# Performance work log

Measured on AMD Instinct MI355X. Metric: run time of the kernel, lower is better.

The kernel has to match this reference:

```python
import jax, jax.numpy as jnp
import numpy as np

EPS = 1e-5


def conv1x1(x, w, b):
    # x: [b,c,h,w], w: [o,c], b: [o] -> [b,o,h,w]  (1x1 conv == channel matmul)
    return jnp.einsum('bchw,oc->bohw', x, w) + b[None, :, None, None]


def nor_mean_std(x):
    # instance norm over spatial dims (torch calc_mean_std uses unbiased var)
    mean = jnp.mean(x, axis=(2, 3), keepdims=True)
    var = jnp.var(x, axis=(2, 3), keepdims=True, ddof=1)
    return (x - mean) / jnp.sqrt(var + EPS)


def nor_mean(x):
    mean = jnp.mean(x, axis=(2, 3), keepdims=True)
    return x - mean, mean


def net(x, w1, b1, w2, b2):
    return conv1x1(jax.nn.relu(conv1x1(x, w1, b1)), w2, b2)


def setup_inputs() -> dict:
    key = jax.random.key(0)
    ks = jax.random.split(key, 8)
    B, C, H, W = 8, 256, 128, 128
    return {
        'content': jax.random.normal(ks[0], (B, C, H, W), jnp.float32),
        'style': jax.random.normal(ks[1], (B, C, H, W), jnp.float32),
        'w1': jax.random.normal(ks[2], (128, 256), jnp.float32) * 0.05,
        'b1': jax.random.normal(ks[3], (128,), jnp.float32) * 0.05,
        'w2': jax.random.normal(ks[4], (32, 128), jnp.float32) * 0.05,
        'b2': jax.random.normal(ks[5], (32,), jnp.float32) * 0.05,
        'wu': jax.random.normal(ks[6], (256, 32), jnp.float32) * 0.05,
        'bu': jax.random.normal(ks[7], (256,), jnp.float32) * 0.05,
    }


def reference(content, style, w1, b1, w2, b2, wu, bu):
    cF_nor = nor_mean_std(content)
    sF_nor, smean = nor_mean(style)
    cF = net(cF_nor, w1, b1, w2, b2)          # [b,32,h,w]
    sF = net(sF_nor, w1, b1, w2, b2)          # [b,32,h,w]
    b, c, h, w = cF.shape
    hw = h * w
    sf = sF.reshape(b, c, hw)
    # channel covariance: [b,32,32]
    s_cov = jnp.einsum('bcn,bdn->bcd', sf, sf) / hw
    s_cov = jax.nn.softmax(s_cov, axis=-1) * (c ** -0.5)
    gF = jnp.einsum('bcd,bdn->bcn', s_cov, cF.reshape(b, c, hw)).reshape(b, c, h, w)
    gF = conv1x1(gF, wu, bu)                  # [b,256,h,w]
    return gF + smean + content
```

## Files before the change

kernel.cpp:

```cpp
#include <hip/hip_runtime.h>

#define HW 16384
#define C_IN 256
#define C_MID 128
#define C_OUT 32
#define EPSF 1e-5f

typedef __bf16 bf16x8 __attribute__((ext_vector_type(8)));
typedef __bf16 bf16x4 __attribute__((ext_vector_type(4)));
typedef float f32x4 __attribute__((ext_vector_type(4)));

__device__ __forceinline__ bf16x4 cvt4(f32x4 v) {
    bf16x4 r;
    r[0] = (__bf16)v[0]; r[1] = (__bf16)v[1];
    r[2] = (__bf16)v[2]; r[3] = (__bf16)v[3];
    return r;
}

__global__ __launch_bounds__(512) void k_stats_s(const float* __restrict__ style,
                                                 float* __restrict__ smean,
                                                 __bf16* __restrict__ sbf) {
    const int bc = blockIdx.x;
    const int t = threadIdx.x;
    const f32x4* sp = (const f32x4*)(style + (size_t)bc * HW);
    const int phase = (bc * 257) & 4095;

    int idx[8];
    #pragma unroll
    for (int i = 0; i < 8; ++i) idx[i] = (phase + t + i * 512) & 4095;

    f32x4 s[8];
    #pragma unroll
    for (int i = 0; i < 8; ++i) s[i] = __builtin_nontemporal_load(sp + idx[i]);
    asm volatile("" ::
        "v"(s[0]), "v"(s[1]), "v"(s[2]), "v"(s[3]),
        "v"(s[4]), "v"(s[5]), "v"(s[6]), "v"(s[7]));

    {
        bf16x4* sb = (bf16x4*)(sbf + (size_t)bc * HW);
        #pragma unroll
        for (int i = 0; i < 8; ++i) sb[idx[i]] = cvt4(s[i]);
    }

    f32x4 a01 = s[0] + s[1], a23 = s[2] + s[3], a45 = s[4] + s[5], a67 = s[6] + s[7];
    f32x4 a = (a01 + a23) + (a45 + a67);
    float ss = (a[0] + a[1]) + (a[2] + a[3]);

    #pragma unroll
    for (int d = 32; d > 0; d >>= 1) ss += __shfl_xor(ss, d, 64);
    __shared__ float rss[8];
    const int wv = t >> 6;
    if ((t & 63) == 0) rss[wv] = ss;
    __syncthreads();
    if (t == 0) {
        float S = 0.f;
        #pragma unroll
        for (int i = 0; i < 8; ++i) S += rss[i];
        smean[bc] = S / (float)HW;
    }
}

__global__ __launch_bounds__(512) void k_stats_c(const float* __restrict__ content,
                                                 float* __restrict__ cmean,
                                                 float* __restrict__ crstd,
                                                 __bf16* __restrict__ cbf) {
    const int bc = blockIdx.x;
    const int t = threadIdx.x;
    const f32x4* cp = (const f32x4*)(content + (size_t)bc * HW);
    const int phase = (bc * 257) & 4095;

    int idx[8];
    #pragma unroll
    for (int i = 0; i < 8; ++i) idx[i] = (phase + t + i * 512) & 4095;

    f32x4 c[8];
    #pragma unroll
    for (int i = 0; i < 8; ++i) c[i] = __builtin_nontemporal_load(cp + idx[i]);
    asm volatile("" ::
        "v"(c[0]), "v"(c[1]), "v"(c[2]), "v"(c[3]),
        "v"(c[4]), "v"(c[5]), "v"(c[6]), "v"(c[7]));

    {
        bf16x4* cb = (bf16x4*)(cbf + (size_t)bc * HW);
        #pragma unroll
        for (int i = 0; i < 8; ++i) cb[idx[i]] = cvt4(c[i]);
    }

    f32x4 a01 = c[0] + c[1], a23 = c[2] + c[3], a45 = c[4] + c[5], a67 = c[6] + c[7];
    f32x4 a = (a01 + a23) + (a45 + a67);
    float cs = (a[0] + a[1]) + (a[2] + a[3]);
    f32x4 q01 = c[0]*c[0] + c[1]*c[1], q23 = c[2]*c[2] + c[3]*c[3];
    f32x4 q45 = c[4]*c[4] + c[5]*c[5], q67 = c[6]*c[6] + c[7]*c[7];
    f32x4 q = (q01 + q23) + (q45 + q67);
    float cq = (q[0] + q[1]) + (q[2] + q[3]);

    #pragma unroll
    for (int d = 32; d > 0; d >>= 1) {
        cs += __shfl_xor(cs, d, 64);
        cq += __shfl_xor(cq, d, 64);
    }
    __shared__ float rs[8], rq[8];
    const int wv = t >> 6;
    if ((t & 63) == 0) { rs[wv] = cs; rq[wv] = cq; }
    __syncthreads();
    if (t == 0) {
        float S = 0.f, Q = 0.f;
        #pragma unroll
        for (int i = 0; i < 8; ++i) { S += rs[i]; Q += rq[i]; }
        float n = (float)HW;
        float var = (Q - S * S / n) / (n - 1.f);
        cmean[bc] = S / n;
        crstd[bc] = 1.f / sqrtf(var + EPSF);
    }
}

__global__ __launch_bounds__(256) void k_wprep_s(const float* __restrict__ w1,
                                                 const float* __restrict__ b1,
                                                 const float* __restrict__ w2,
                                                 const float* __restrict__ smean,
                                                 __bf16* __restrict__ W1s,
                                                 float* __restrict__ bias1s,
                                                 __bf16* __restrict__ W2b) {
    int o = blockIdx.x, b = blockIdx.y, t = threadIdx.x;
    float w = w1[o * 256 + t];
    if (b == 0) {
        W1s[o * 256 + t] = (__bf16)w;
        if (t < 32) W2b[o * 32 + t] = (__bf16)w2[o * 32 + t];
    }
    float ps = w * smean[b * 256 + t];
    __shared__ float rB[256];
    rB[t] = ps;
    __syncthreads();
    for (int off = 128; off > 0; off >>= 1) {
        if (t < off) rB[t] += rB[t + off];
        __syncthreads();
    }
    if (t == 0) bias1s[b * 128 + o] = b1[o] - rB[0];
}

__global__ __launch_bounds__(256) void k_wprep_c(const float* __restrict__ w1,
                                                 const float* __restrict__ b1,
                                                 const float* __restrict__ cmean,
                                                 const float* __restrict__ crstd,
                                                 __bf16* __restrict__ W1c,
                                                 float* __restrict__ bias1c) {
    int o = blockIdx.x, b = blockIdx.y, t = threadIdx.x;
    float w = w1[o * 256 + t];
    float r = crstd[b * 256 + t];
    float wc = w * r;
    W1c[((size_t)(b * 128 + o)) * 256 + t] = (__bf16)wc;
    float pc = wc * cmean[b * 256 + t];
    __shared__ float rA[256];
    rA[t] = pc;
    __syncthreads();
    for (int off = 128; off > 0; off >>= 1) {
        if (t < off) rA[t] += rA[t + off];
        __syncthreads();
    }
    if (t == 0) bias1c[b * 128 + o] = b1[o] - rA[0];
}

__device__ __forceinline__ void stage_tile(const __bf16* __restrict__ xb,
                                           int p0, int tid, __bf16* Xl) {
    const int c = tid;
    const __bf16* src = xb + (size_t)c * HW + p0;
    bf16x8 v[8];
    #pragma unroll
    for (int j = 0; j < 8; ++j) v[j] = *(const bf16x8*)(src + j * 8);
    char* base = (char*)Xl;
    #pragma unroll
    for (int j = 0; j < 8; ++j) {
        #pragma unroll
        for (int e = 0; e < 8; ++e)
            *(__bf16*)(base + (j * 8 + e) * 512 + ((2 * c) ^ (e << 4))) = v[j][e];
    }
}

__global__ __launch_bounds__(256) void k_net_s(const __bf16* __restrict__ x,
                                               const __bf16* __restrict__ W1,
                                               const float* __restrict__ bias1,
                                               const __bf16* __restrict__ W2,
                                               const float* __restrict__ b2,
                                               float* __restrict__ partial) {
    __shared__ __bf16 Xl[64 * 256];
    __shared__ __bf16 Tl[64 * 128];
    const int tid = threadIdx.x;
    const int l = tid & 63, wv = tid >> 6;
    const int lr = l & 15, g = l >> 4;
    const int sw = (lr & 7) << 4;
    const int p0 = blockIdx.x * 64;
    const int b = blockIdx.y;
    const __bf16* xb = x + (size_t)b * C_IN * HW;

    stage_tile(xb, p0, tid, Xl);
    __syncthreads();

    const f32x4 zero4 = {0.f, 0.f, 0.f, 0.f};
    f32x4 acc[2][4];
    #pragma unroll
    for (int mt = 0; mt < 2; ++mt)
        #pragma unroll
        for (int nt = 0; nt < 4; ++nt) acc[mt][nt] = zero4;

    const __bf16* wrow0 = W1 + (size_t)(wv * 32 + lr) * 256 + g * 8;
    const __bf16* wrow1 = wrow0 + 16 * 256;

    #pragma unroll
    for (int kt = 0; kt < 8; ++kt) {
        bf16x8 a0 = *(const bf16x8*)(wrow0 + kt * 32);
        bf16x8 a1 = *(const bf16x8*)(wrow1 + kt * 32);
        #pragma unroll
        for (int nt = 0; nt < 4; ++nt) {
            const char* xrow = (const char*)&Xl[(nt * 16 + lr) * 256];
            bf16x8 bfr = *(const bf16x8*)(xrow + (((kt * 32 + g * 8) * 2) ^ sw));
            acc[0][nt] = __builtin_amdgcn_mfma_f32_16x16x32_bf16(a0, bfr, acc[0][nt], 0, 0, 0);
            acc[1][nt] = __builtin_amdgcn_mfma_f32_16x16x32_bf16(a1, bfr, acc[1][nt], 0, 0, 0);
        }
    }

    float4 bia[2];
    bia[0] = *(const float4*)&bias1[b * 128 + wv * 32 + g * 4];
    bia[1] = *(const float4*)&bias1[b * 128 + wv * 32 + 16 + g * 4];
    __syncthreads();
    #pragma unroll
    for (int mt = 0; mt < 2; ++mt) {
        #pragma unroll
        for (int nt = 0; nt < 4; ++nt) {
            const int p = nt * 16 + lr;
            char* trow = (char*)&Tl[p * 128];
            const int ob = (wv * 32 + mt * 16 + g * 4) * 2;
            bf16x4 tv;
            tv[0] = (__bf16)fmaxf(acc[mt][nt][0] + bia[mt].x, 0.f);
            tv[1] = (__bf16)fmaxf(acc[mt][nt][1] + bia[mt].y, 0.f);
            tv[2] = (__bf16)fmaxf(acc[mt][nt][2] + bia[mt].z, 0.f);
            tv[3] = (__bf16)fmaxf(acc[mt][nt][3] + bia[mt].w, 0.f);
            *(bf16x4*)(trow + (ob ^ sw)) = tv;
        }
    }
    __syncthreads();

    f32x4 acc2[2];
    acc2[0] = zero4; acc2[1] = zero4;
    const int p = wv * 16 + lr;
    const char* trow = (const char*)&Tl[p * 128];
    const __bf16* w2r0 = W2 + (size_t)lr * 128 + g * 8;
    const __bf16* w2r1 = w2r0 + 16 * 128;
    #pragma unroll
    for (int kt = 0; kt < 4; ++kt) {
        bf16x8 bfr = *(const bf16x8*)(trow + (((kt * 32 + g * 8) * 2) ^ sw));
        bf16x8 a0 = *(const bf16x8*)(w2r0 + kt * 32);
        bf16x8 a1 = *(const bf16x8*)(w2r1 + kt * 32);
        acc2[0] = __builtin_amdgcn_mfma_f32_16x16x32_bf16(a0, bfr, acc2[0], 0, 0, 0);
        acc2[1] = __builtin_amdgcn_mfma_f32_16x16x32_bf16(a1, bfr, acc2[1], 0, 0, 0);
    }
    float4 bb0 = *(const float4*)&b2[g * 4];
    float4 bb1 = *(const float4*)&b2[16 + g * 4];
    const int o0 = g * 4;

    float* gt = (float*)Xl;
    gt[(o0 + 0) * 65 + p] = acc2[0][0] + bb0.x;
    gt[(o0 + 1) * 65 + p] = acc2[0][1] + bb0.y;
    gt[(o0 + 2) * 65 + p] = acc2[0][2] + bb0.z;
    gt[(o0 + 3) * 65 + p] = acc2[0][3] + bb0.w;
    gt[(16 + o0 + 0) * 65 + p] = acc2[1][0] + bb1.x;
    gt[(16 + o0 + 1) * 65 + p] = acc2[1][1] + bb1.y;
    gt[(16 + o0 + 2) * 65 + p] = acc2[1][2] + bb1.z;
    gt[(16 + o0 + 3) * 65 + p] = acc2[1][3] + bb1.w;
    __syncthreads();
    const int gi = tid >> 3, jb = (tid & 7) * 4;
    float g4[4] = {0.f, 0.f, 0.f, 0.f};
    #pragma unroll 8
    for (int n = 0; n < 64; ++n) {
        float si = gt[gi * 65 + n];
        #pragma unroll
        for (int q = 0; q < 4; ++q)
            g4[q] = fmaf(si, gt[(jb + q) * 65 + n], g4[q]);
    }
    float* dst = partial + ((size_t)(b * 256 + blockIdx.x)) * 1024 + tid * 4;
    #pragma unroll
    for (int q = 0; q < 4; ++q) dst[q] = g4[q];
}

__global__ __launch_bounds__(1024) void k_softmax2(const float* __restrict__ partial,
                                                   float* __restrict__ scov) {
    int b = blockIdx.x;
    int j = threadIdx.x, i = threadIdx.y;
    const float* base = partial + (size_t)b * 256 * 1024 + i * 32 + j;
    float v0 = 0.f, v1 = 0.f, v2 = 0.f, v3 = 0.f;
    #pragma unroll 4
    for (int s = 0; s < 256; s += 4) {
        v0 += base[(s + 0) * 1024];
        v1 += base[(s + 1) * 1024];
        v2 += base[(s + 2) * 1024];
        v3 += base[(s + 3) * 1024];
    }
    float v = ((v0 + v1) + (v2 + v3)) * (1.f / (float)HW);
    float m = v;
    #pragma unroll
    for (int d = 16; d > 0; d >>= 1) m = fmaxf(m, __shfl_xor(m, d, 32));
    float e = expf(v - m);
    float sum = e;
    #pragma unroll
    for (int d = 16; d > 0; d >>= 1) sum += __shfl_xor(sum, d, 32);
    scov[(size_t)b * 1024 + i * 32 + j] = e / sum * 0.17677669529663687f;
}

__global__ __launch_bounds__(256) void k_netc_final(const __bf16* __restrict__ x,
                                                    const __bf16* __restrict__ W1,
                                                    const float* __restrict__ bias1,
                                                    const __bf16* __restrict__ W2,
                                                    const float* __restrict__ b2,
                                                    const float* __restrict__ scov,
                                                    const float* __restrict__ wu,
                                                    const float* __restrict__ bu,
                                                    const float* __restrict__ smean,
                                                    float* __restrict__ out) {
    __shared__ __bf16 Xl[64 * 256];
    __shared__ __bf16 Tl[64 * 128];
    __shared__ float sCov[1024];
    __shared__ float sG[32 * 64];
    const int tid = threadIdx.x;
    const int l = tid & 63, wv = tid >> 6;
    const int lr = l & 15, g = l >> 4;
    const int sw = (lr & 7) << 4;
    const int p0 = blockIdx.x * 64;
    const int b = blockIdx.y;
    const __bf16* xb = x + (size_t)b * C_IN * HW;

    #pragma unroll
    for (int q = 0; q < 4; ++q)
        sCov[tid + 256 * q] = scov[(size_t)b * 1024 + tid + 256 * q];
    stage_tile(xb, p0, tid, Xl);
    __syncthreads();

    const f32x4 zero4 = {0.f, 0.f, 0.f, 0.f};
    f32x4 acc1[2][4];
    #pragma unroll
    for (int mt = 0; mt < 2; ++mt)
        #pragma unroll
        for (int nt = 0; nt < 4; ++nt) acc1[mt][nt] = zero4;

    const __bf16* W1b = W1 + ((size_t)b << 15);
    const __bf16* wrow0 = W1b + (size_t)(wv * 32 + lr) * 256 + g * 8;
    const __bf16* wrow1 = wrow0 + 16 * 256;

    #pragma unroll
    for (int kt = 0; kt < 8; ++kt) {
        bf16x8 a0 = *(const bf16x8*)(wrow0 + kt * 32);
        bf16x8 a1 = *(const bf16x8*)(wrow1 + kt * 32);
        #pragma unroll
        for (int nt = 0; nt < 4; ++nt) {
            const char* xrow = (const char*)&Xl[(nt * 16 + lr) * 256];
            bf16x8 bfr = *(const bf16x8*)(xrow + (((kt * 32 + g * 8) * 2) ^ sw));
            acc1[0][nt] = __builtin_amdgcn_mfma_f32_16x16x32_bf16(a0, bfr, acc1[0][nt], 0, 0, 0);
            acc1[1][nt] = __builtin_amdgcn_mfma_f32_16x16x32_bf16(a1, bfr, acc1[1][nt], 0, 0, 0);
        }
    }

    float4 bia[2];
    bia[0] = *(const float4*)&bias1[b * 128 + wv * 32 + g * 4];
    bia[1] = *(const float4*)&bias1[b * 128 + wv * 32 + 16 + g * 4];
    #pragma unroll
    for (int mt = 0; mt < 2; ++mt) {
        #pragma unroll
        for (int nt = 0; nt < 4; ++nt) {
            const int p = nt * 16 + lr;
            char* trow = (char*)&Tl[p * 128];
            const int ob = (wv * 32 + mt * 16 + g * 4) * 2;
            bf16x4 tv;
            tv[0] = (__bf16)fmaxf(acc1[mt][nt][0] + bia[mt].x, 0.f);
            tv[1] = (__bf16)fmaxf(acc1[mt][nt][1] + bia[mt].y, 0.f);
            tv[2] = (__bf16)fmaxf(acc1[mt][nt][2] + bia[mt].z, 0.f);
            tv[3] = (__bf16)fmaxf(acc1[mt][nt][3] + bia[mt].w, 0.f);
            *(bf16x4*)(trow + (ob ^ sw)) = tv;
        }
    }
    __syncthreads();

    f32x4 acc2[2];
    acc2[0] = zero4; acc2[1] = zero4;
    const int p = wv * 16 + lr;
    {
        const char* trow = (const char*)&Tl[p * 128];
        const __bf16* w2r0 = W2 + (size_t)lr * 128 + g * 8;
        const __bf16* w2r1 = w2r0 + 16 * 128;
        #pragma unroll
        for (int kt = 0; kt < 4; ++kt) {
            bf16x8 bfr = *(const bf16x8*)(trow + (((kt * 32 + g * 8) * 2) ^ sw));
            bf16x8 a0 = *(const bf16x8*)(w2r0 + kt * 32);
            bf16x8 a1 = *(const bf16x8*)(w2r1 + kt * 32);
            acc2[0] = __builtin_amdgcn_mfma_f32_16x16x32_bf16(a0, bfr, acc2[0], 0, 0, 0);
            acc2[1] = __builtin_amdgcn_mfma_f32_16x16x32_bf16(a1, bfr, acc2[1], 0, 0, 0);
        }
    }
    float4 bb0 = *(const float4*)&b2[g * 4];
    float4 bb1 = *(const float4*)&b2[16 + g * 4];
    const int o0 = g * 4;

    __syncthreads();
    float* sC = (float*)Tl;
    sC[(o0 + 0) * 64 + p] = acc2[0][0] + bb0.x;
    sC[(o0 + 1) * 64 + p] = acc2[0][1] + bb0.y;
    sC[(o0 + 2) * 64 + p] = acc2[0][2] + bb0.z;
    sC[(o0 + 3) * 64 + p] = acc2[0][3] + bb0.w;
    sC[(16 + o0 + 0) * 64 + p] = acc2[1][0] + bb1.x;
    sC[(16 + o0 + 1) * 64 + p] = acc2[1][1] + bb1.y;
    sC[(16 + o0 + 2) * 64 + p] = acc2[1][2] + bb1.z;
    sC[(16 + o0 + 3) * 64 + p] = acc2[1][3] + bb1.w;
    __syncthreads();

    {
        int gp = tid & 63, gib = (tid >> 6) * 8;
        #pragma unroll
        for (int rr = 0; rr < 8; ++rr) {
            int gi = gib + rr;
            float a = 0.f;
            #pragma unroll
            for (int k = 0; k < 32; ++k)
                a = fmaf(sCov[gi * 32 + k], sC[k * 64 + gp], a);
            sG[gi * 64 + gp] = a;
        }
    }
    __syncthreads();

    const int tx = tid & 7, ty = tid >> 3;
    const float* wurow = wu + (size_t)(ty * 8) * 32;
    float acc[8][8];
    #pragma unroll
    for (int i = 0; i < 8; ++i)
        #pragma unroll
        for (int j = 0; j < 8; ++j) acc[i][j] = 0.f;
    #pragma unroll 4
    for (int k = 0; k < 32; ++k) {
        float a[8];
        #pragma unroll
        for (int i = 0; i < 8; ++i) a[i] = wurow[i * 32 + k];
        float4 b4a = *(const float4*)&sG[k * 64 + tx * 8];
        float4 b4b = *(const float4*)&sG[k * 64 + tx * 8 + 4];
        float bb[8] = {b4a.x, b4a.y, b4a.z, b4a.w, b4b.x, b4b.y, b4b.z, b4b.w};
        #pragma unroll
        for (int i = 0; i < 8; ++i)
            #pragma unroll
            for (int j = 0; j < 8; ++j)
                acc[i][j] = fmaf(a[i], bb[j], acc[i][j]);
    }
    float cvv[8][8];
    #pragma unroll
    for (int j = 0; j < 8; ++j) {
        const int pl = tx * 8 + j;
        bf16x8 rv = *(const bf16x8*)((const char*)Xl + pl * 512 + ((ty * 16) ^ (j << 4)));
        #pragma unroll
        for (int i = 0; i < 8; ++i) cvv[i][j] = (float)rv[i];
    }
    #pragma unroll
    for (int i = 0; i < 8; ++i) {
        int o = ty * 8 + i;
        float add = bu[o] + smean[b * 256 + o];
        float* dst = out + (size_t)b * C_IN * HW + (size_t)o * HW + p0 + tx * 8;
        f32x4 r0 = {acc[i][0] + add + cvv[i][0], acc[i][1] + add + cvv[i][1],
                    acc[i][2] + add + cvv[i][2], acc[i][3] + add + cvv[i][3]};
        f32x4 r1 = {acc[i][4] + add + cvv[i][4], acc[i][5] + add + cvv[i][5],
                    acc[i][6] + add + cvv[i][6], acc[i][7] + add + cvv[i][7]};
        __builtin_nontemporal_store(r0, (f32x4*)dst);
        __builtin_nontemporal_store(r1, (f32x4*)(dst + 4));
    }
}

extern "C" void kernel_launch(void* const* d_in, const int* in_sizes, int n_in,
                              void* d_out, int out_size, void* d_ws, size_t ws_size,
                              hipStream_t stream) {
    const float* content = (const float*)d_in[0];
    const float* style   = (const float*)d_in[1];
    const float* w1      = (const float*)d_in[2];
    const float* b1      = (const float*)d_in[3];
    const float* w2      = (const float*)d_in[4];
    const float* b2      = (const float*)d_in[5];
    const float* wu      = (const float*)d_in[6];
    const float* bu      = (const float*)d_in[7];
    float* out = (float*)d_out;
    float* ws  = (float*)d_ws;

    float* cmean   = ws;
    float* crstd   = ws + 2048;
    float* smean   = ws + 4096;
    float* scov    = ws + 6144;
    float* bias1c  = ws + 14336;
    float* bias1s  = ws + 15360;
    __bf16* W2b    = (__bf16*)(ws + 16384);
    __bf16* W1s    = (__bf16*)(ws + 18432);
    __bf16* W1c    = (__bf16*)(ws + 34816);
    float* partial = ws + 165888;
    __bf16* cbf    = (__bf16*)(ws + 2263040);
    __bf16* sbf    = (__bf16*)(ws + 19040256);

    k_stats_s<<<dim3(2048), 512, 0, stream>>>(style, smean, sbf);
    k_wprep_s<<<dim3(128, 8), 256, 0, stream>>>(w1, b1, w2, smean, W1s, bias1s, W2b);
    k_net_s<<<dim3(256, 8), 256, 0, stream>>>(sbf, W1s, bias1s, W2b, b2, partial);
    k_softmax2<<<dim3(8), dim3(32, 32), 0, stream>>>(partial, scov);
    k_stats_c<<<dim3(2048), 512, 0, stream>>>(content, cmean, crstd, cbf);
    k_wprep_c<<<dim3(128, 8), 256, 0, stream>>>(w1, b1, cmean, crstd, W1c, bias1c);
    k_netc_final<<<dim3(256, 8), 256, 0, stream>>>(cbf, W1c, bias1c, W2b, b2,
                                                   scov, wu, bu, smean, out);
}
```

Measured before the change: 225.9 us.

## Double-buffer K-chunked input tiles in final kernel to cut LDS and overlap loads

The fused final kernel no longer stages the whole 64x256 bf16 input tile in shared memory. It streams 64-channel chunks through two 8 KB buffers, prefetching the next chunk into registers while MFMAs run on the current one. That drops shared memory to about 45 KB, and launch bounds now request 3 blocks per CU to raise occupancy. The residual add rereads the bf16 input from global memory instead of shared memory. The costs are extra barriers per chunk, 16 scalar 2-byte transposing shared stores per thread, and a second global read of the tile.

```diff
diff --git a/kernel.cpp b/kernel.cpp
--- a/kernel.cpp
+++ b/kernel.cpp
@@ -305,20 +305,23 @@
     scov[(size_t)b * 1024 + i * 32 + j] = e / sum * 0.17677669529663687f;
 }
 
-__global__ __launch_bounds__(256) void k_netc_final(const __bf16* __restrict__ x,
-                                                    const __bf16* __restrict__ W1,
-                                                    const float* __restrict__ bias1,
-                                                    const __bf16* __restrict__ W2,
-                                                    const float* __restrict__ b2,
-                                                    const float* __restrict__ scov,
-                                                    const float* __restrict__ wu,
-                                                    const float* __restrict__ bu,
-                                                    const float* __restrict__ smean,
-                                                    float* __restrict__ out) {
-    __shared__ __bf16 Xl[64 * 256];
-    __shared__ __bf16 Tl[64 * 128];
-    __shared__ float sCov[1024];
-    __shared__ float sG[32 * 64];
+__global__ __launch_bounds__(256, 3) void k_netc_final(const __bf16* __restrict__ x,
+                                                       const __bf16* __restrict__ W1,
+                                                       const float* __restrict__ bias1,
+                                                       const __bf16* __restrict__ W2,
+                                                       const float* __restrict__ b2,
+                                                       const float* __restrict__ scov,
+                                                       const float* __restrict__ wu,
+                                                       const float* __restrict__ bu,
+                                                       const float* __restrict__ smean,
+                                                       float* __restrict__ out) {
+    __shared__ char smem[45056];
+    __bf16* Xb[2] = {(__bf16*)smem, (__bf16*)(smem + 8192)};
+    __bf16* Tl  = (__bf16*)(smem + 16384);
+    float* sCov = (float*)(smem + 32768);
+    float* sG   = (float*)(smem + 36864);
+    float* sC   = (float*)(smem + 16384);
+
     const int tid = threadIdx.x;
     const int l = tid & 63, wv = tid >> 6;
     const int lr = l & 15, g = l >> 4;
@@ -327,10 +330,30 @@
     const int b = blockIdx.y;
     const __bf16* xb = x + (size_t)b * C_IN * HW;
 
+    const int cl = tid & 63;
+    const int pq = (tid >> 6) * 16;
+
     #pragma unroll
     for (int q = 0; q < 4; ++q)
         sCov[tid + 256 * q] = scov[(size_t)b * 1024 + tid + 256 * q];
-    stage_tile(xb, p0, tid, Xl);
+
+    bf16x8 stg0, stg1;
+    {
+        const __bf16* src = xb + (size_t)cl * HW + p0 + pq;
+        stg0 = *(const bf16x8*)src;
+        stg1 = *(const bf16x8*)(src + 8);
+        char* base = (char*)Xb[0];
+        #pragma unroll
+        for (int e = 0; e < 8; ++e) {
+            int p = pq + e;
+            *(__bf16*)(base + p * 128 + ((2 * cl) ^ ((p & 7) << 4))) = stg0[e];
+        }
+        #pragma unroll
+        for (int e = 0; e < 8; ++e) {
+            int p = pq + 8 + e;
+            *(__bf16*)(base + p * 128 + ((2 * cl) ^ ((p & 7) << 4))) = stg1[e];
+        }
+    }
     __syncthreads();
 
     const f32x4 zero4 = {0.f, 0.f, 0.f, 0.f};
@@ -341,19 +364,42 @@
         for (int nt = 0; nt < 4; ++nt) acc1[mt][nt] = zero4;
 
     const __bf16* W1b = W1 + ((size_t)b << 15);
-    const __bf16* wrow0 = W1b + (size_t)(wv * 32 + lr) * 256 + g * 8;
-    const __bf16* wrow1 = wrow0 + 16 * 256;
-
-    #pragma unroll
-    for (int kt = 0; kt < 8; ++kt) {
-        bf16x8 a0 = *(const bf16x8*)(wrow0 + kt * 32);
-        bf16x8 a1 = *(const bf16x8*)(wrow1 + kt * 32);
-        #pragma unroll
-        for (int nt = 0; nt < 4; ++nt) {
-            const char* xrow = (const char*)&Xl[(nt * 16 + lr) * 256];
-            bf16x8 bfr = *(const bf16x8*)(xrow + (((kt * 32 + g * 8) * 2) ^ sw));
-            acc1[0][nt] = __builtin_amdgcn_mfma_f32_16x16x32_bf16(a0, bfr, acc1[0][nt], 0, 0, 0);
-            acc1[1][nt] = __builtin_amdgcn_mfma_f32_16x16x32_bf16(a1, bfr, acc1[1][nt], 0, 0, 0);
+    const __bf16* wbase = W1b + (size_t)(wv * 32 + lr) * 256 + g * 8;
+
+    #pragma unroll
+    for (int kc = 0; kc < 4; ++kc) {
+        const __bf16* cur = Xb[kc & 1];
+        if (kc < 3) {
+            const __bf16* src = xb + (size_t)((kc + 1) * 64 + cl) * HW + p0 + pq;
+            stg0 = *(const bf16x8*)src;
+            stg1 = *(const bf16x8*)(src + 8);
+        }
+        #pragma unroll
+        for (int kt = 0; kt < 2; ++kt) {
+            const __bf16* w0 = wbase + kc * 64 + kt * 32;
+            bf16x8 a0 = *(const bf16x8*)w0;
+            bf16x8 a1 = *(const bf16x8*)(w0 + 16 * 256);
+            #pragma unroll
+            for (int nt = 0; nt < 4; ++nt) {
+                const char* xrow = (const char*)cur + (nt * 16 + lr) * 128;
+                bf16x8 bfr = *(const bf16x8*)(xrow + (((kt * 32 + g * 8) * 2) ^ sw));
+                acc1[0][nt] = __builtin_amdgcn_mfma_f32_16x16x32_bf16(a0, bfr, acc1[0][nt], 0, 0, 0);
+                acc1[1][nt] = __builtin_amdgcn_mfma_f32_16x16x32_bf16(a1, bfr, acc1[1][nt], 0, 0, 0);
+            }
+        }
+        if (kc < 3) {
+            char* base = (char*)Xb[(kc + 1) & 1];
+            #pragma unroll
+            for (int e = 0; e < 8; ++e) {
+                int p = pq + e;
+                *(__bf16*)(base + p * 128 + ((2 * cl) ^ ((p & 7) << 4))) = stg0[e];
+            }
+            #pragma unroll
+            for (int e = 0; e < 8; ++e) {
+                int p = pq + 8 + e;
+                *(__bf16*)(base + p * 128 + ((2 * cl) ^ ((p & 7) << 4))) = stg1[e];
+            }
+            __syncthreads();
         }
     }
 
@@ -398,7 +444,6 @@
     const int o0 = g * 4;
 
     __syncthreads();
-    float* sC = (float*)Tl;
     sC[(o0 + 0) * 64 + p] = acc2[0][0] + bb0.x;
     sC[(o0 + 1) * 64 + p] = acc2[0][1] + bb0.y;
     sC[(o0 + 2) * 64 + p] = acc2[0][2] + bb0.z;
@@ -444,23 +489,17 @@
             for (int j = 0; j < 8; ++j)
                 acc[i][j] = fmaf(a[i], bb[j], acc[i][j]);
     }
-    float cvv[8][8];
-    #pragma unroll
-    for (int j = 0; j < 8; ++j) {
-        const int pl = tx * 8 + j;
-        bf16x8 rv = *(const bf16x8*)((const char*)Xl + pl * 512 + ((ty * 16) ^ (j << 4)));
-        #pragma unroll
-        for (int i = 0; i < 8; ++i) cvv[i][j] = (float)rv[i];
-    }
     #pragma unroll
     for (int i = 0; i < 8; ++i) {
         int o = ty * 8 + i;
         float add = bu[o] + smean[b * 256 + o];
+        const __bf16* csrc = xb + (size_t)o * HW + p0 + tx * 8;
+        bf16x8 rv = *(const bf16x8*)csrc;
         float* dst = out + (size_t)b * C_IN * HW + (size_t)o * HW + p0 + tx * 8;
-        f32x4 r0 = {acc[i][0] + add + cvv[i][0], acc[i][1] + add + cvv[i][1],
-                    acc[i][2] + add + cvv[i][2], acc[i][3] + add + cvv[i][3]};
-        f32x4 r1 = {acc[i][4] + add + cvv[i][4], acc[i][5] + add + cvv[i][5],
-                    acc[i][6] + add + cvv[i][6], acc[i][7] + add + cvv[i][7]};
+        f32x4 r0 = {acc[i][0] + add + (float)rv[0], acc[i][1] + add + (float)rv[1],
+                    acc[i][2] + add + (float)rv[2], acc[i][3] + add + (float)rv[3]};
+        f32x4 r1 = {acc[i][4] + add + (float)rv[4], acc[i][5] + add + (float)rv[5],
+                    acc[i][6] + add + (float)rv[6], acc[i][7] + add + (float)rv[7]};
         __builtin_nontemporal_store(r0, (f32x4*)dst);
         __builtin_nontemporal_store(r1, (f32x4*)(dst + 4));
     }
```

Result: no change. 226.9 us (+0.5%).
